# Optimization experiments

Measured on AMD Instinct MI355X. Metric: run time of the kernel, lower is better.

## Reference

```python
import jax, jax.numpy as jnp
import numpy as np
import math

B, N, E, H = 16, 1024, 512, 8
DH = E // H

def setup_inputs() -> dict:
    key = jax.random.key(0)
    ks = jax.random.split(key, 12)
    inp = {
        "q": jax.random.normal(ks[0], (B, N, E), dtype=jnp.float32),
        "k": jax.random.normal(ks[1], (B, N, E), dtype=jnp.float32),
        "v": jax.random.normal(ks[2], (B, N, E), dtype=jnp.float32),
        "d": jax.random.uniform(ks[3], (B, N, N), dtype=jnp.float32),
        # nn.Linear weights (out, in) with orthogonal-ish init scaled small, zero bias
        "Wq": jax.random.normal(ks[4], (E, E), dtype=jnp.float32) * 0.01,
        "bq": jnp.zeros((E,), dtype=jnp.float32),
        "Wk": jax.random.normal(ks[5], (E, E), dtype=jnp.float32) * 0.01,
        "bk": jnp.zeros((E,), dtype=jnp.float32),
        "Wv": jax.random.normal(ks[6], (E, E), dtype=jnp.float32) * 0.01,
        "bv": jnp.zeros((E,), dtype=jnp.float32),
        "Wp": jax.random.normal(ks[7], (E, E), dtype=jnp.float32) * 0.01,
        "bp": jnp.zeros((E,), dtype=jnp.float32),
    }
    return inp

def _heads(x, W, b):
    # torch Linear: x @ W.T + b, then split heads -> [B, H, N, DH]
    y = jnp.einsum('bne,fe->bnf', x, W) + b
    return y.reshape(x.shape[0], x.shape[1], H, DH).transpose(0, 2, 1, 3)

def reference(q, k, v, d, Wq, bq, Wk, bk, Wv, bv, Wp, bp):
    qh = _heads(q, Wq, bq)                                  # [B,H,N,DH]
    kh = _heads(k, Wk, bk)
    vh = _heads(v, Wv, bv)
    scale = 1.0 / math.sqrt(DH)
    att = jnp.einsum('bhnd,bhmd->bhnm', qh, kh) * scale     # [B,H,N,N]
    db = d[:, None, :, :]                                   # broadcast over heads
    att = jax.nn.softmax(att + db, axis=-1)
    att = att * db                                          # multiplicative distance bias post-softmax
    x = jnp.einsum('bhnm,bhmd->bhnd', att, vh)              # [B,H,N,DH]
    x = x.transpose(0, 2, 1, 3).reshape(q.shape[0], q.shape[1], E)
    return jnp.einsum('bne,fe->bnf', x, Wp) + bp
```

## Files before the change

### kernel.cpp

```cpp
#include <hip/hip_runtime.h>
#include <hip/hip_bf16.h>


#define Bc  16
#define Nc  1024
#define Ec  512
#define Hc  8
#define DHc 64

typedef float  f32x4  __attribute__((ext_vector_type(4)));
typedef int    i32x4  __attribute__((ext_vector_type(4)));
typedef short  s16x4  __attribute__((ext_vector_type(4)));
typedef short  s16x8  __attribute__((ext_vector_type(8)));
typedef __bf16 bf16x8 __attribute__((ext_vector_type(8)));

static __device__ __forceinline__ f32x4 mfma16(s16x8 a, s16x8 b, f32x4 c) {
    return __builtin_amdgcn_mfma_f32_16x16x32_bf16(
        __builtin_bit_cast(bf16x8, a), __builtin_bit_cast(bf16x8, b), c, 0, 0, 0);
}

static __device__ __forceinline__ unsigned short f2bf(float f) {
    return __builtin_bit_cast(unsigned short, __float2bfloat16(f));
}

static __device__ __forceinline__ s16x8 pack_bf16(f32x4 a, f32x4 b) {
    s16x8 r;
    r[0] = (short)f2bf(a[0]); r[1] = (short)f2bf(a[1]);
    r[2] = (short)f2bf(a[2]); r[3] = (short)f2bf(a[3]);
    r[4] = (short)f2bf(b[0]); r[5] = (short)f2bf(b[1]);
    r[6] = (short)f2bf(b[2]); r[7] = (short)f2bf(b[3]);
    return r;
}

static __device__ __forceinline__ void gld16(const void* g, void* l) {
    __builtin_amdgcn_global_load_lds(
        (const __attribute__((address_space(1))) void*)g,
        (__attribute__((address_space(3))) void*)l, 16, 0, 0);
}

static __device__ __forceinline__ void lds_publish_barrier() {
    asm volatile("s_waitcnt lgkmcnt(0)" ::: "memory");
    __builtin_amdgcn_s_barrier();
    asm volatile("" ::: "memory");
}

__global__ __launch_bounds__(256) void wcvt_kernel(
    const float* __restrict__ Wq, const float* __restrict__ Wk,
    const float* __restrict__ Wv, const float* __restrict__ Wp,
    unsigned short* __restrict__ wbf)
{
    const int seg = blockIdx.x >> 7;
    const float* src = seg == 0 ? Wq : (seg == 1 ? Wk : (seg == 2 ? Wv : Wp));
    const int g = (blockIdx.x & 127) * 256 + threadIdx.x;
    const float* p = src + (size_t)g * 8;
    f32x4 a = *(const f32x4*)p, b = *(const f32x4*)(p + 4);
    *(s16x8*)(wbf + (size_t)seg * 262144 + (size_t)g * 8) = pack_bf16(a, b);
}

__global__ __launch_bounds__(256) void proj3_kernel(
    const float* __restrict__ qi, const float* __restrict__ ki,
    const float* __restrict__ vi, const unsigned short* __restrict__ wbf,
    const float* __restrict__ bq, const float* __restrict__ bk,
    const float* __restrict__ bv,
    unsigned short* __restrict__ qo, unsigned short* __restrict__ ko,
    unsigned short* __restrict__ vo)
{
    const int z = blockIdx.z;
    const float* Af = z == 0 ? qi : (z == 1 ? ki : vi);
    const unsigned short* Wb = wbf + (size_t)z * 262144;
    const float* bias = z == 0 ? bq : (z == 1 ? bk : bv);
    unsigned short* out = z == 0 ? qo : (z == 1 ? ko : vo);
    const int mode = (z == 2) ? 1 : 0;

    __shared__ unsigned short Asb[128 * 32];
    __shared__ unsigned short Bsb[128 * 32];

    const int tid = threadIdx.x;
    const int w = tid >> 6, lane = tid & 63;
    const int lr = lane & 15, grp = lane >> 4;
    const int wr = w >> 1, wc = w & 1;
    const int m0 = blockIdx.x * 128, n0 = blockIdx.y * 128;

    f32x4 acc[4][4];
#pragma unroll
    for (int i = 0; i < 4; ++i)
#pragma unroll
        for (int j = 0; j < 4; ++j) acc[i][j] = (f32x4)(0.0f);

    const int arow = tid >> 2, aslot = tid & 3;
    const int acol = ((aslot ^ (arow & 3)) << 3);
    const int h4 = lane >> 2, l4 = lane & 3;
    const int bcol = ((l4 ^ (h4 & 3)) << 3);
    const int ob = ((grp ^ (lr & 3)) << 3);

    for (int k0 = 0; k0 < Ec; k0 += 32) {
        __syncthreads();
        f32x4 a0[2], a1[2];
#pragma unroll
        for (int i = 0; i < 2; ++i) {
            const float* p = Af + (size_t)(m0 + i * 64 + arow) * Ec + k0 + acol;
            a0[i] = *(const f32x4*)p;
            a1[i] = *(const f32x4*)(p + 4);
        }
#pragma unroll
        for (int i = 0; i < 2; ++i) {
            const int chunk = i * 4 + w;
            const int row = chunk * 16 + h4;
            gld16(Wb + (size_t)(n0 + row) * Ec + k0 + bcol,
                  (char*)Bsb + chunk * 1024 + lane * 16);
        }
#pragma unroll
        for (int i = 0; i < 2; ++i)
            *reinterpret_cast<s16x8*>((char*)Asb + i * 4096 + tid * 16) =
                pack_bf16(a0[i], a1[i]);
        __syncthreads();

        s16x8 afr[4], bfr[4];
#pragma unroll
        for (int mi = 0; mi < 4; ++mi)
            afr[mi] = *(const s16x8*)(Asb + (wr * 64 + mi * 16 + lr) * 32 + ob);
#pragma unroll
        for (int ni = 0; ni < 4; ++ni)
            bfr[ni] = *(const s16x8*)(Bsb + (wc * 64 + ni * 16 + lr) * 32 + ob);
#pragma unroll
        for (int mi = 0; mi < 4; ++mi)
#pragma unroll
            for (int ni = 0; ni < 4; ++ni)
                acc[mi][ni] = mfma16(afr[mi], bfr[ni], acc[mi][ni]);
    }

#pragma unroll
    for (int mi = 0; mi < 4; ++mi) {
        const int mbase = m0 + wr * 64 + mi * 16 + grp * 4;
#pragma unroll
        for (int ni = 0; ni < 4; ++ni) {
            const int f = n0 + wc * 64 + ni * 16 + lr;
            const float bi = bias[f];
            f32x4 vv = acc[mi][ni];
            const int hh = f >> 6, dh = f & 63;
            if (mode == 0) {
#pragma unroll
                for (int r = 0; r < 4; ++r) {
                    const int m = mbase + r;
                    out[(((size_t)(m >> 10) * Hc + hh) * Nc + (m & (Nc - 1))) * DHc + dh] =
                        f2bf(vv[r] + bi);
                }
            } else {
                const int bb = mbase >> 10, n = mbase & (Nc - 1);
                s16x4 pk;
#pragma unroll
                for (int r = 0; r < 4; ++r) pk[r] = (short)f2bf(vv[r] + bi);
                *(s16x4*)&out[(((size_t)bb * Hc + hh) * DHc + dh) * Nc + n] = pk;
            }
        }
    }
}

__global__ __launch_bounds__(256) void outproj_kernel(
    const unsigned short* __restrict__ Ab, const unsigned short* __restrict__ Wb,
    const float* __restrict__ bias, float* __restrict__ out)
{
    __shared__ unsigned short Asb[128 * 32];
    __shared__ unsigned short Bsb[128 * 32];

    const int tid = threadIdx.x;
    const int w = tid >> 6, lane = tid & 63;
    const int lr = lane & 15, grp = lane >> 4;
    const int wr = w >> 1, wc = w & 1;
    const int m0 = blockIdx.x * 128, n0 = blockIdx.y * 128;

    f32x4 acc[4][4];
#pragma unroll
    for (int i = 0; i < 4; ++i)
#pragma unroll
        for (int j = 0; j < 4; ++j) acc[i][j] = (f32x4)(0.0f);

    const int h4 = lane >> 2, l4 = lane & 3;
    const int bcol = ((l4 ^ (h4 & 3)) << 3);
    const int ob = ((grp ^ (lr & 3)) << 3);

    for (int k0 = 0; k0 < Ec; k0 += 32) {
        __syncthreads();
#pragma unroll
        for (int i = 0; i < 2; ++i) {
            const int chunk = i * 4 + w;
            const int row = chunk * 16 + h4;
            gld16(Ab + (size_t)(m0 + row) * Ec + k0 + bcol,
                  (char*)Asb + chunk * 1024 + lane * 16);
            gld16(Wb + (size_t)(n0 + row) * Ec + k0 + bcol,
                  (char*)Bsb + chunk * 1024 + lane * 16);
        }
        __syncthreads();

        s16x8 afr[4], bfr[4];
#pragma unroll
        for (int mi = 0; mi < 4; ++mi)
            afr[mi] = *(const s16x8*)(Asb + (wr * 64 + mi * 16 + lr) * 32 + ob);
#pragma unroll
        for (int ni = 0; ni < 4; ++ni)
            bfr[ni] = *(const s16x8*)(Bsb + (wc * 64 + ni * 16 + lr) * 32 + ob);
#pragma unroll
        for (int mi = 0; mi < 4; ++mi)
#pragma unroll
            for (int ni = 0; ni < 4; ++ni)
                acc[mi][ni] = mfma16(afr[mi], bfr[ni], acc[mi][ni]);
    }

#pragma unroll
    for (int mi = 0; mi < 4; ++mi) {
        const int mbase = m0 + wr * 64 + mi * 16 + grp * 4;
#pragma unroll
        for (int ni = 0; ni < 4; ++ni) {
            const int f = n0 + wc * 64 + ni * 16 + lr;
            const float bi = bias[f];
            f32x4 vv = acc[mi][ni];
#pragma unroll
            for (int r = 0; r < 4; ++r)
                out[(size_t)(mbase + r) * Ec + f] = vv[r] + bi;
        }
    }
}

__global__ __launch_bounds__(256) void attn_kernel(
    const unsigned short* __restrict__ qh, const unsigned short* __restrict__ kh,
    const unsigned short* __restrict__ vt, const float* __restrict__ dmat,
    unsigned short* __restrict__ xh)
{
    __shared__ unsigned short K_lds[2][64 * 64];
    __shared__ unsigned short V_lds[2][64 * 64];
    __shared__ unsigned short P_lds[4][32][72];

    const int lin = blockIdx.x;
    const int j = lin >> 3;
    const int h = j & 7;
    const int qt = (j >> 3) & 7;
    const int b = ((lin & 7) << 1) | (j >> 6);

    const int tid = threadIdx.x;
    const int w = tid >> 6, lane = tid & 63;
    const int lr = lane & 15, grp = lane >> 4;
    const int h8 = lane >> 3, l8 = lane & 7;
    const int q0 = qt * 128;
    const int bh = b * Hc + h;
    const int qw = q0 + w * 32;
    const int kofs = grp * 4;
    const int scol = (l8 ^ h8) * 8;
    const float* dbase0 = dmat + ((size_t)b * Nc + qw + lr) * Nc;
    const float* dbase1 = dbase0 + (size_t)16 * Nc;

    const float LOG2E = 1.4426950408889634f;
    const float SC    = 0.125f * LOG2E;
    const float MC    = -4.0f * LOG2E;

    s16x8 bq0[2], bq1[2];
#pragma unroll
    for (int ks = 0; ks < 2; ++ks) {
        bq0[ks] = *reinterpret_cast<const s16x8*>(
            qh + ((size_t)bh * Nc + qw + lr) * DHc + ks * 32 + grp * 8);
        bq1[ks] = *reinterpret_cast<const s16x8*>(
            qh + ((size_t)bh * Nc + qw + 16 + lr) * DHc + ks * 32 + grp * 8);
    }

    f32x4 acc0[4], acc1[4];
#pragma unroll
    for (int c = 0; c < 4; ++c) { acc0[c] = (f32x4)(0.0f); acc1[c] = (f32x4)(0.0f); }
    float lsum0 = 0.f, lsum1 = 0.f;

    const int NT = Nc / 64;
    i32x4 kst[2], vst[2];
#pragma unroll
    for (int i = 0; i < 2; ++i) {
        const int ch = w + i * 4;
        kst[i] = *reinterpret_cast<const i32x4*>(
            kh + ((size_t)bh * Nc + ch * 8 + h8) * DHc + scol);
        vst[i] = *reinterpret_cast<const i32x4*>(
            vt + ((size_t)bh * DHc + ch * 8 + h8) * Nc + scol);
    }
#pragma unroll
    for (int i = 0; i < 2; ++i) {
        const int ch = w + i * 4;
        *reinterpret_cast<i32x4*>((char*)K_lds[0] + ch * 1024 + lane * 16) = kst[i];
        *reinterpret_cast<i32x4*>((char*)V_lds[0] + ch * 1024 + lane * 16) = vst[i];
    }
#pragma unroll
    for (int i = 0; i < 2; ++i) {
        const int ch = w + i * 4;
        kst[i] = *reinterpret_cast<const i32x4*>(
            kh + ((size_t)bh * Nc + 64 + ch * 8 + h8) * DHc + scol);
        vst[i] = *reinterpret_cast<const i32x4*>(
            vt + ((size_t)bh * DHc + ch * 8 + h8) * Nc + 64 + scol);
    }
    f32x4 dv0[4], dv1[4];
#pragma unroll
    for (int c = 0; c < 4; ++c) {
        dv0[c] = *reinterpret_cast<const f32x4*>(dbase0 + c * 16 + kofs);
        dv1[c] = *reinterpret_cast<const f32x4*>(dbase1 + c * 16 + kofs);
    }

    for (int kt = 0; kt < NT; ++kt) {
        const int cur = kt & 1;
        lds_publish_barrier();
        if (kt + 1 < NT) {
#pragma unroll
            for (int i = 0; i < 2; ++i) {
                const int ch = w + i * 4;
                *reinterpret_cast<i32x4*>((char*)K_lds[cur ^ 1] + ch * 1024 + lane * 16) = kst[i];
                *reinterpret_cast<i32x4*>((char*)V_lds[cur ^ 1] + ch * 1024 + lane * 16) = vst[i];
            }
        }
        if (kt + 2 < NT) {
            const int k2 = (kt + 2) * 64;
#pragma unroll
            for (int i = 0; i < 2; ++i) {
                const int ch = w + i * 4;
                kst[i] = *reinterpret_cast<const i32x4*>(
                    kh + ((size_t)bh * Nc + k2 + ch * 8 + h8) * DHc + scol);
                vst[i] = *reinterpret_cast<const i32x4*>(
                    vt + ((size_t)bh * DHc + ch * 8 + h8) * Nc + k2 + scol);
            }
        }

        f32x4 lgt0[4], lgt1[4];
#pragma unroll
        for (int c = 0; c < 4; ++c) { lgt0[c] = (f32x4)(0.0f); lgt1[c] = (f32x4)(0.0f); }
        __builtin_amdgcn_s_setprio(1);
#pragma unroll
        for (int ks = 0; ks < 2; ++ks) {
#pragma unroll
            for (int c = 0; c < 4; ++c) {
                const int row = c * 16 + lr;
                const int slot = (4 * ks + grp) ^ (lr & 7);
                s16x8 ak = *reinterpret_cast<const s16x8*>(
                    (const char*)K_lds[cur] + row * 128 + slot * 16);
                lgt0[c] = mfma16(ak, bq0[ks], lgt0[c]);
                lgt1[c] = mfma16(ak, bq1[ks], lgt1[c]);
            }
        }
        __builtin_amdgcn_s_setprio(0);
#pragma unroll
        for (int c = 0; c < 4; ++c) {
            s16x4 pk0, pk1;
#pragma unroll
            for (int r = 0; r < 4; ++r) {
                const float dl0 = fmaf(dv0[c][r], LOG2E, MC);
                const float p0 = __builtin_amdgcn_exp2f(fmaf(lgt0[c][r], SC, dl0));
                lsum0 += p0;
                pk0[r] = (short)f2bf(p0 * dv0[c][r]);
                const float dl1 = fmaf(dv1[c][r], LOG2E, MC);
                const float p1 = __builtin_amdgcn_exp2f(fmaf(lgt1[c][r], SC, dl1));
                lsum1 += p1;
                pk1[r] = (short)f2bf(p1 * dv1[c][r]);
            }
            *reinterpret_cast<s16x4*>(&P_lds[w][lr][c * 16 + kofs]) = pk0;
            *reinterpret_cast<s16x4*>(&P_lds[w][16 + lr][c * 16 + kofs]) = pk1;
        }
        if (kt + 1 < NT) {
            const int k1 = (kt + 1) * 64;
#pragma unroll
            for (int c = 0; c < 4; ++c) {
                dv0[c] = *reinterpret_cast<const f32x4*>(dbase0 + k1 + c * 16 + kofs);
                dv1[c] = *reinterpret_cast<const f32x4*>(dbase1 + k1 + c * 16 + kofs);
            }
        }
        __builtin_amdgcn_s_setprio(1);
#pragma unroll
        for (int ks = 0; ks < 2; ++ks) {
            s16x8 pa0 = *reinterpret_cast<const s16x8*>(&P_lds[w][lr][ks * 32 + grp * 8]);
            s16x8 pa1 = *reinterpret_cast<const s16x8*>(&P_lds[w][16 + lr][ks * 32 + grp * 8]);
#pragma unroll
            for (int c = 0; c < 4; ++c) {
                const int row = c * 16 + lr;
                const int slot = (4 * ks + grp) ^ (lr & 7);
                s16x8 bv = *reinterpret_cast<const s16x8*>(
                    (const char*)V_lds[cur] + row * 128 + slot * 16);
                acc0[c] = mfma16(pa0, bv, acc0[c]);
                acc1[c] = mfma16(pa1, bv, acc1[c]);
            }
        }
        __builtin_amdgcn_s_setprio(0);
    }
    lsum0 += __shfl_xor(lsum0, 16, 64);
    lsum0 += __shfl_xor(lsum0, 32, 64);
    lsum1 += __shfl_xor(lsum1, 16, 64);
    lsum1 += __shfl_xor(lsum1, 32, 64);
    const float invd0 = 1.0f / lsum0, invd1 = 1.0f / lsum1;
    float inv0[4], inv1[4];
#pragma unroll
    for (int r = 0; r < 4; ++r) {
        inv0[r] = __shfl(invd0, grp * 4 + r, 64);
        inv1[r] = __shfl(invd1, grp * 4 + r, 64);
    }
#pragma unroll
    for (int c = 0; c < 4; ++c)
#pragma unroll
        for (int r = 0; r < 4; ++r) {
            xh[((size_t)b * Nc + qw + grp * 4 + r) * Ec + h * DHc + c * 16 + lr] =
                f2bf(acc0[c][r] * inv0[r]);
            xh[((size_t)b * Nc + qw + 16 + grp * 4 + r) * Ec + h * DHc + c * 16 + lr] =
                f2bf(acc1[c][r] * inv1[r]);
        }
}

extern "C" void kernel_launch(void* const* d_in, const int* in_sizes, int n_in,
                              void* d_out, int out_size, void* d_ws, size_t ws_size,
                              hipStream_t stream)
{
    (void)in_sizes; (void)n_in; (void)out_size; (void)ws_size;
    const float* q  = (const float*)d_in[0];
    const float* k  = (const float*)d_in[1];
    const float* v  = (const float*)d_in[2];
    const float* dm = (const float*)d_in[3];
    const float* Wq = (const float*)d_in[4];
    const float* bq = (const float*)d_in[5];
    const float* Wk = (const float*)d_in[6];
    const float* bk = (const float*)d_in[7];
    const float* Wv = (const float*)d_in[8];
    const float* bv = (const float*)d_in[9];
    const float* Wp = (const float*)d_in[10];
    const float* bp = (const float*)d_in[11];
    float* out = (float*)d_out;

    const size_t sz = (size_t)Bc * Hc * Nc * DHc;
    unsigned short* qhb = (unsigned short*)d_ws;
    unsigned short* khb = qhb + sz;
    unsigned short* vtb = khb + sz;
    unsigned short* xhb = vtb + sz;
    unsigned short* wbf = xhb + sz;

    wcvt_kernel<<<dim3(512), dim3(256), 0, stream>>>(Wq, Wk, Wv, Wp, wbf);
    proj3_kernel<<<dim3(Bc * Nc / 128, Ec / 128, 3), dim3(256), 0, stream>>>(
        q, k, v, wbf, bq, bk, bv, qhb, khb, vtb);
    attn_kernel<<<dim3(Bc * Hc * Nc / 128), dim3(256), 0, stream>>>(
        qhb, khb, vtb, dm, xhb);
    outproj_kernel<<<dim3(Bc * Nc / 128, Ec / 128), dim3(256), 0, stream>>>(
        xhb, wbf + (size_t)3 * 262144, bp, out);
}
```

Measured before the change: 157.5 us.

## Process two heads per attention block so they share distance-matrix loads

The attention block grows to 512 threads covering two heads of the same batch and query tile. Each half of the block owns its own K/V LDS buffer, which replaces the previous double buffering with a single buffer per head. Grouping two heads per block is meant to improve cache reuse of the large distance matrix, which is shared across heads, and to raise the number of waves per block. The cost is that K/V prefetch now hides only one tile ahead, and each tile needs two barriers per iteration across 8 waves.

```diff
diff --git a/kernel.cpp b/kernel.cpp
--- a/kernel.cpp
+++ b/kernel.cpp
@@ -40,6 +40,11 @@
 
 static __device__ __forceinline__ void lds_publish_barrier() {
     asm volatile("s_waitcnt lgkmcnt(0)" ::: "memory");
+    __builtin_amdgcn_s_barrier();
+    asm volatile("" ::: "memory");
+}
+static __device__ __forceinline__ void plain_barrier() {
+    asm volatile("" ::: "memory");
     __builtin_amdgcn_s_barrier();
     asm volatile("" ::: "memory");
 }
@@ -221,28 +226,30 @@
     }
 }
 
-__global__ __launch_bounds__(256) void attn_kernel(
+__global__ __launch_bounds__(512) void attn_kernel(
     const unsigned short* __restrict__ qh, const unsigned short* __restrict__ kh,
     const unsigned short* __restrict__ vt, const float* __restrict__ dmat,
     unsigned short* __restrict__ xh)
 {
     __shared__ unsigned short K_lds[2][64 * 64];
     __shared__ unsigned short V_lds[2][64 * 64];
-    __shared__ unsigned short P_lds[4][32][72];
+    __shared__ unsigned short P_lds[8][32][72];
 
     const int lin = blockIdx.x;
     const int j = lin >> 3;
-    const int h = j & 7;
-    const int qt = (j >> 3) & 7;
-    const int b = ((lin & 7) << 1) | (j >> 6);
+    const int hp = j & 3;
+    const int qt = (j >> 2) & 7;
+    const int b = ((lin & 7) << 1) | (j >> 5);
 
     const int tid = threadIdx.x;
     const int w = tid >> 6, lane = tid & 63;
+    const int w4 = w & 3, hh = w >> 2;
     const int lr = lane & 15, grp = lane >> 4;
     const int h8 = lane >> 3, l8 = lane & 7;
     const int q0 = qt * 128;
+    const int h = hp * 2 + hh;
     const int bh = b * Hc + h;
-    const int qw = q0 + w * 32;
+    const int qw = q0 + w4 * 32;
     const int kofs = grp * 4;
     const int scol = (l8 ^ h8) * 8;
     const float* dbase0 = dmat + ((size_t)b * Nc + qw + lr) * Nc;
@@ -270,26 +277,12 @@
     i32x4 kst[2], vst[2];
 #pragma unroll
     for (int i = 0; i < 2; ++i) {
-        const int ch = w + i * 4;
+        const int ch = w4 + i * 4;
         kst[i] = *reinterpret_cast<const i32x4*>(
             kh + ((size_t)bh * Nc + ch * 8 + h8) * DHc + scol);
         vst[i] = *reinterpret_cast<const i32x4*>(
             vt + ((size_t)bh * DHc + ch * 8 + h8) * Nc + scol);
     }
-#pragma unroll
-    for (int i = 0; i < 2; ++i) {
-        const int ch = w + i * 4;
-        *reinterpret_cast<i32x4*>((char*)K_lds[0] + ch * 1024 + lane * 16) = kst[i];
-        *reinterpret_cast<i32x4*>((char*)V_lds[0] + ch * 1024 + lane * 16) = vst[i];
-    }
-#pragma unroll
-    for (int i = 0; i < 2; ++i) {
-        const int ch = w + i * 4;
-        kst[i] = *reinterpret_cast<const i32x4*>(
-            kh + ((size_t)bh * Nc + 64 + ch * 8 + h8) * DHc + scol);
-        vst[i] = *reinterpret_cast<const i32x4*>(
-            vt + ((size_t)bh * DHc + ch * 8 + h8) * Nc + 64 + scol);
-    }
     f32x4 dv0[4], dv1[4];
 #pragma unroll
     for (int c = 0; c < 4; ++c) {
@@ -298,27 +291,24 @@
     }
 
     for (int kt = 0; kt < NT; ++kt) {
-        const int cur = kt & 1;
+#pragma unroll
+        for (int i = 0; i < 2; ++i) {
+            const int ch = w4 + i * 4;
+            *reinterpret_cast<i32x4*>((char*)K_lds[hh] + ch * 1024 + lane * 16) = kst[i];
+            *reinterpret_cast<i32x4*>((char*)V_lds[hh] + ch * 1024 + lane * 16) = vst[i];
+        }
+        if (kt + 1 < NT) {
+            const int k1 = (kt + 1) * 64;
+#pragma unroll
+            for (int i = 0; i < 2; ++i) {
+                const int ch = w4 + i * 4;
+                kst[i] = *reinterpret_cast<const i32x4*>(
+                    kh + ((size_t)bh * Nc + k1 + ch * 8 + h8) * DHc + scol);
+                vst[i] = *reinterpret_cast<const i32x4*>(
+                    vt + ((size_t)bh * DHc + ch * 8 + h8) * Nc + k1 + scol);
+            }
+        }
         lds_publish_barrier();
-        if (kt + 1 < NT) {
-#pragma unroll
-            for (int i = 0; i < 2; ++i) {
-                const int ch = w + i * 4;
-                *reinterpret_cast<i32x4*>((char*)K_lds[cur ^ 1] + ch * 1024 + lane * 16) = kst[i];
-                *reinterpret_cast<i32x4*>((char*)V_lds[cur ^ 1] + ch * 1024 + lane * 16) = vst[i];
-            }
-        }
-        if (kt + 2 < NT) {
-            const int k2 = (kt + 2) * 64;
-#pragma unroll
-            for (int i = 0; i < 2; ++i) {
-                const int ch = w + i * 4;
-                kst[i] = *reinterpret_cast<const i32x4*>(
-                    kh + ((size_t)bh * Nc + k2 + ch * 8 + h8) * DHc + scol);
-                vst[i] = *reinterpret_cast<const i32x4*>(
-                    vt + ((size_t)bh * DHc + ch * 8 + h8) * Nc + k2 + scol);
-            }
-        }
 
         f32x4 lgt0[4], lgt1[4];
 #pragma unroll
@@ -331,7 +321,7 @@
                 const int row = c * 16 + lr;
                 const int slot = (4 * ks + grp) ^ (lr & 7);
                 s16x8 ak = *reinterpret_cast<const s16x8*>(
-                    (const char*)K_lds[cur] + row * 128 + slot * 16);
+                    (const char*)K_lds[hh] + row * 128 + slot * 16);
                 lgt0[c] = mfma16(ak, bq0[ks], lgt0[c]);
                 lgt1[c] = mfma16(ak, bq1[ks], lgt1[c]);
             }
@@ -372,12 +362,13 @@
                 const int row = c * 16 + lr;
                 const int slot = (4 * ks + grp) ^ (lr & 7);
                 s16x8 bv = *reinterpret_cast<const s16x8*>(
-                    (const char*)V_lds[cur] + row * 128 + slot * 16);
+                    (const char*)V_lds[hh] + row * 128 + slot * 16);
                 acc0[c] = mfma16(pa0, bv, acc0[c]);
                 acc1[c] = mfma16(pa1, bv, acc1[c]);
             }
         }
         __builtin_amdgcn_s_setprio(0);
+        plain_barrier();
     }
     lsum0 += __shfl_xor(lsum0, 16, 64);
     lsum0 += __shfl_xor(lsum0, 32, 64);
@@ -430,7 +421,7 @@
     wcvt_kernel<<<dim3(512), dim3(256), 0, stream>>>(Wq, Wk, Wv, Wp, wbf);
     proj3_kernel<<<dim3(Bc * Nc / 128, Ec / 128, 3), dim3(256), 0, stream>>>(
         q, k, v, wbf, bq, bk, bv, qhb, khb, vtb);
-    attn_kernel<<<dim3(Bc * Hc * Nc / 128), dim3(256), 0, stream>>>(
+    attn_kernel<<<dim3(Bc * Hc * Nc / 256), dim3(512), 0, stream>>>(
         qhb, khb, vtb, dm, xhb);
     outproj_kernel<<<dim3(Bc * Nc / 128, Ec / 128), dim3(256), 0, stream>>>(
         xhb, wbf + (size_t)3 * 262144, bp, out);
```

Result: slower. 166.3 us (+5.6%).
